# Performance work log

Hardware: AMD Instinct MI355X
Metric: run time of the kernel (lower is better)

The kernel has to match this reference:

```python
import jax, jax.numpy as jnp
import numpy as np


def _fake_quant(w):
    # Dynamic per-tensor int8 quantization of weights (scale = max|w|/127),
    # immediately dequantized, as quantized_lstm does for its packed weights.
    s = jnp.max(jnp.abs(w)) / 127.0
    q = jnp.clip(jnp.round(w / s), -128.0, 127.0) * s
    # straight-through so the same code is usable under vjp
    return w + jax.lax.stop_gradient(q - w)


def _run_dir(xs, h0, c0, w_ih, w_hh, b, reverse):
    # xs: [T,B,in]; h0,c0: [B,H]; w_ih: [4H,in]; w_hh: [4H,H]; b: [4H]
    def step(carry, x_t):
        h, c = carry
        gates = x_t @ w_ih.T + h @ w_hh.T + b  # [B,4H]
        i, f, g, o = jnp.split(gates, 4, axis=-1)  # PyTorch gate order i,f,g,o
        c = jax.nn.sigmoid(f) * c + jax.nn.sigmoid(i) * jnp.tanh(g)
        h = jax.nn.sigmoid(o) * jnp.tanh(c)
        return (h, c), h
    (hT, cT), ys = jax.lax.scan(step, (h0, c0), xs, reverse=reverse)
    return ys, hT, cT


def _lstm(x, h0, c0, w_ih, w_hh, b_ih, b_hh):
    # x: [B,T,I] (batch_first); h0/c0: [L*2,B,H]; weights stacked [L,2,...]
    L = w_ih.shape[0]
    xs = jnp.transpose(x, (1, 0, 2))  # time-major [T,B,I]
    h_n, c_n = [], []
    for l in range(L):
        outs = []
        for d in range(2):  # 0=fwd, 1=bwd
            idx = 2 * l + d
            wih = _fake_quant(w_ih[l, d])
            whh = _fake_quant(w_hh[l, d])
            b = b_ih[l, d] + b_hh[l, d]
            ys, hT, cT = _run_dir(xs, h0[idx], c0[idx], wih, whh, b, reverse=(d == 1))
            outs.append(ys)
            h_n.append(hT)
            c_n.append(cT)
        xs = jnp.concatenate(outs, axis=-1)  # [T,B,2H] feeds next layer
    out = jnp.transpose(xs, (1, 0, 2))  # back to batch_first [B,T,2H]
    return out, jnp.stack(h_n), jnp.stack(c_n)


def setup_inputs() -> dict:
    key = jax.random.key(0)
    ks = jax.random.split(key, 7)
    B, T, I, H, L = 32, 256, 1024, 512, 2
    sc = 1.0 / np.sqrt(H)
    return {
        "x": jax.random.normal(ks[0], (B, T, I), jnp.float32),
        "h0": jax.random.normal(ks[1], (2 * L, B, H), jnp.float32),
        "c0": jax.random.normal(ks[2], (2 * L, B, H), jnp.float32),
        "w_ih": jax.random.normal(ks[3], (L, 2, 4 * H, I), jnp.float32) * sc,
        "w_hh": jax.random.normal(ks[4], (L, 2, 4 * H, H), jnp.float32) * sc,
        "b_ih": jax.random.normal(ks[5], (L, 2, 4 * H), jnp.float32) * sc,
        "b_hh": jax.random.normal(ks[6], (L, 2, 4 * H), jnp.float32) * sc,
    }


def reference(x, h0, c0, w_ih, w_hh, b_ih, b_hh):
    return _lstm(x, h0, c0, w_ih, w_hh, b_ih, b_hh)
```

## Files before the change

kernel.cpp:

```cpp
#include <hip/hip_runtime.h>

typedef __attribute__((ext_vector_type(8))) short bf16x8;
typedef __attribute__((ext_vector_type(4))) float f32x4;
typedef __attribute__((ext_vector_type(4))) unsigned u32x4;

#define BB   32
#define TT   256
#define II   1024
#define HH   512
#define GG   2048
#define BT   8192

#define WS_OFF_FLAGS   0ull
#define WS_OFF_SCALES  1024ull
#define WS_MEMSET_SPAN 2048ull
#define WS_OFF_QIH     4096ull
#define QIH_BYTES      (4ull*GG*II*2)
#define WS_OFF_QHH     (WS_OFF_QIH + QIH_BYTES)
#define QHH_BYTES      (4ull*GG*HH*2)
#define WS_OFF_XBUF    (WS_OFF_QHH + QHH_BYTES)
#define XBUF_BYTES     (1ull*BT*II*2)
#define WS_OFF_YS1     (WS_OFF_XBUF + XBUF_BYTES)
#define WS_OFF_HBUF    (WS_OFF_YS1 + XBUF_BYTES)
#define HBUF_BYTES     (2ull*2*BB*HH*2)
#define WS_OFF_GX      (WS_OFF_HBUF + HBUF_BYTES)
#define GX_ELEMS       (2ull*TT*GG*BB)

__device__ __forceinline__ unsigned short f2bf(float f){
  unsigned u = __float_as_uint(f);
  u += 0x7fffu + ((u >> 16) & 1u);
  return (unsigned short)(u >> 16);
}
__device__ __forceinline__ float bf2f(unsigned short h){ return __uint_as_float(((unsigned)h) << 16); }
__device__ __forceinline__ unsigned pack2(float a, float b){ return (unsigned)f2bf(a) | ((unsigned)f2bf(b) << 16); }
__device__ __forceinline__ float sigm(float x){ return 1.0f / (1.0f + __expf(-x)); }
__device__ __forceinline__ float tanh_(float x){
  float e = __expf(-2.0f * fabsf(x));
  float t = (1.0f - e) / (1.0f + e);
  return x < 0.0f ? -t : t;
}

__device__ __forceinline__ void st_short(void* p, unsigned v){
  asm volatile("global_store_short %0, %1, off" :: "v"(p), "v"(v) : "memory");
}
__device__ __forceinline__ void st_short_coh(void* p, unsigned v){
  asm volatile("global_store_short %0, %1, off sc0 sc1" :: "v"(p), "v"(v) : "memory");
}
__device__ __forceinline__ void st_dword(void* p, float v){
  asm volatile("global_store_dword %0, %1, off" :: "v"(p), "v"(v) : "memory");
}
__device__ __forceinline__ void ld_dword(float* d, const void* p){
  asm volatile("global_load_dword %0, %1, off" : "=v"(*d) : "v"(p));
}
__device__ __forceinline__ void ld_ushort(unsigned* d, const void* p){
  asm volatile("global_load_ushort %0, %1, off" : "=v"(*d) : "v"(p));
}
__device__ __forceinline__ void ld_b128_coh(u32x4* d, const void* p){
  asm volatile("global_load_dwordx4 %0, %1, off sc0 sc1" : "=v"(*d) : "v"(p));
}
__device__ __forceinline__ void ld_b128(bf16x8* d, const void* p){
  asm volatile("global_load_dwordx4 %0, %1, off" : "=v"(*d) : "v"(p));
}
#define WAITV0() do{ asm volatile("s_waitcnt vmcnt(0)" ::: "memory"); __builtin_amdgcn_sched_barrier(0); }while(0)
#define WAITL0() do{ asm volatile("s_waitcnt lgkmcnt(0)" ::: "memory"); __builtin_amdgcn_sched_barrier(0); }while(0)

__global__ __launch_bounds__(256) void k_absmax(const float* __restrict__ wih,
                                                const float* __restrict__ whh,
                                                unsigned* __restrict__ scales_raw){
  int t = blockIdx.y;
  const float* base; size_t n;
  if (t < 4){ base = wih + (size_t)t * GG * II; n = (size_t)GG * II; }
  else      { base = whh + (size_t)(t - 4) * GG * HH; n = (size_t)GG * HH; }
  size_t gtid = (size_t)blockIdx.x * 256 + threadIdx.x;
  float m = 0.0f;
  const float4* b4 = (const float4*)base;
  size_t n4 = n >> 2;
  for (size_t i = gtid; i < n4; i += 8192){
    float4 v = b4[i];
    m = fmaxf(m, fmaxf(fmaxf(fabsf(v.x), fabsf(v.y)), fmaxf(fabsf(v.z), fabsf(v.w))));
  }
  for (int off = 32; off; off >>= 1) m = fmaxf(m, __shfl_xor(m, off));
  __shared__ float red[4];
  int w = threadIdx.x >> 6, l = threadIdx.x & 63;
  if (l == 0) red[w] = m;
  __syncthreads();
  if (threadIdx.x == 0){
    m = fmaxf(fmaxf(red[0], red[1]), fmaxf(red[2], red[3]));
    atomicMax(&scales_raw[t], __float_as_uint(m));
  }
}

__global__ __launch_bounds__(256) void k_quant_ih(const float* __restrict__ wih,
                                                  unsigned short* __restrict__ qih,
                                                  const unsigned* __restrict__ scales_raw){
  size_t i8 = (size_t)blockIdx.x * 256 + threadIdx.x;
  int t = (int)(i8 >> 18);
  size_t off = (i8 & 262143) << 3;
  float s = __uint_as_float(scales_raw[t]) / 127.0f;
  s = fmaxf(s, 1e-30f);
  const float* src = wih + ((size_t)t << 21) + off;
  float4 v0 = *(const float4*)src, v1 = *(const float4*)(src + 4);
  float q[8] = {v0.x, v0.y, v0.z, v0.w, v1.x, v1.y, v1.z, v1.w};
#pragma unroll
  for (int j = 0; j < 8; ++j) q[j] = fminf(127.0f, fmaxf(-128.0f, rintf(q[j] / s)));
  uint4 o; o.x = pack2(q[0], q[1]); o.y = pack2(q[2], q[3]); o.z = pack2(q[4], q[5]); o.w = pack2(q[6], q[7]);
  *(uint4*)(qih + ((size_t)t << 21) + off) = o;
}

__global__ __launch_bounds__(256) void k_quant_hh(const float* __restrict__ whh,
                                                  unsigned short* __restrict__ qhh,
                                                  const unsigned* __restrict__ scales_raw){
  size_t i8 = (size_t)blockIdx.x * 256 + threadIdx.x;
  int t = (int)(i8 >> 17);
  size_t o = i8 & 131071;
  int k8 = (int)(o & 63);
  int r  = (int)((o >> 6) & 63);
  int bi = (int)(o >> 12);
  int w = r >> 4, hu = (r >> 2) & 3, gt = r & 3;
  int j = gt * 512 + bi * 16 + w * 4 + hu;
  float s = __uint_as_float(scales_raw[4 + t]) / 127.0f;
  s = fmaxf(s, 1e-30f);
  const float* src = whh + ((size_t)t << 20) + (size_t)j * HH + ((size_t)k8 << 3);
  float4 v0 = *(const float4*)src, v1 = *(const float4*)(src + 4);
  float q[8] = {v0.x, v0.y, v0.z, v0.w, v1.x, v1.y, v1.z, v1.w};
#pragma unroll
  for (int jj = 0; jj < 8; ++jj) q[jj] = fminf(127.0f, fmaxf(-128.0f, rintf(q[jj] / s)));
  uint4 ov; ov.x = pack2(q[0], q[1]); ov.y = pack2(q[2], q[3]); ov.z = pack2(q[4], q[5]); ov.w = pack2(q[6], q[7]);
  *(uint4*)(qhh + ((size_t)t << 20) + (((size_t)bi * 64 + r) << 9) + ((size_t)k8 << 3)) = ov;
}

__global__ __launch_bounds__(256) void k_cvtx(const float* __restrict__ x,
                                              unsigned short* __restrict__ xbuf){
  size_t i8 = (size_t)blockIdx.x * 256 + threadIdx.x;
  size_t row = i8 >> 7;
  int c8 = (int)(i8 & 127);
  int t = (int)(row >> 5), b = (int)(row & 31);
  const float* src = x + (((size_t)b * TT + t) << 10) + ((size_t)c8 << 3);
  float4 v0 = *(const float4*)src, v1 = *(const float4*)(src + 4);
  uint4 o; o.x = pack2(v0.x, v0.y); o.y = pack2(v0.z, v0.w); o.z = pack2(v1.x, v1.y); o.w = pack2(v1.z, v1.w);
  *(uint4*)(xbuf + (row << 10) + ((size_t)c8 << 3)) = o;
}

__global__ __launch_bounds__(256) void k_gemm(const unsigned short* __restrict__ Aq,
                                              const unsigned short* __restrict__ X,
                                              float* __restrict__ gxf,
                                              unsigned short* __restrict__ gxh, int gx16,
                                              const unsigned* __restrict__ scales_raw, int sbase){
  int d = blockIdx.z;
  const unsigned short* A = Aq + ((size_t)d << 21);
  float s = __uint_as_float(scales_raw[sbase + d]) / 127.0f;
  __shared__ unsigned short As[128 * 64];
  __shared__ unsigned short Bs[128 * 64];
  int tid = threadIdx.x;
  int l = tid & 63;
  int wv = tid >> 6;
  int wr = wv >> 1, wc = wv & 1;
  int jt = blockIdx.y, mt = blockIdx.x;
  size_t arow0 = (size_t)jt * 128;
  size_t brow0 = (size_t)mt * 128;
  f32x4 acc[4][4];
  f32x4 z = {0.f, 0.f, 0.f, 0.f};
#pragma unroll
  for (int i = 0; i < 4; ++i)
#pragma unroll
    for (int j = 0; j < 4; ++j) acc[i][j] = z;

  for (int kt = 0; kt < II; kt += 64){
    __syncthreads();
#pragma unroll
    for (int p = 0; p < 4; ++p){
      int ch = p * 256 + tid;
      int r = ch >> 3; int ce = (ch & 7) << 3;
      *(uint4*)&As[r * 64 + ce] = *(const uint4*)&A[(arow0 + r) * II + kt + ce];
      *(uint4*)&Bs[r * 64 + ce] = *(const uint4*)&X[(brow0 + r) * II + kt + ce];
    }
    __syncthreads();
#pragma unroll
    for (int kk = 0; kk < 64; kk += 32){
      bf16x8 a[4], b[4];
#pragma unroll
      for (int mi = 0; mi < 4; ++mi) a[mi] = *(const bf16x8*)&As[(wr * 64 + mi * 16 + (l & 15)) * 64 + kk + (l >> 4) * 8];
#pragma unroll
      for (int ni = 0; ni < 4; ++ni) b[ni] = *(const bf16x8*)&Bs[(wc * 64 + ni * 16 + (l & 15)) * 64 + kk + (l >> 4) * 8];
#pragma unroll
      for (int mi = 0; mi < 4; ++mi)
#pragma unroll
        for (int ni = 0; ni < 4; ++ni)
          acc[mi][ni] = __builtin_amdgcn_mfma_f32_16x16x32_bf16(a[mi], b[ni], acc[mi][ni], 0, 0, 0);
    }
  }
  size_t gxbase = (size_t)d * ((size_t)TT * GG * BB);
#pragma unroll
  for (int mi = 0; mi < 4; ++mi){
    int j0 = jt * 128 + wr * 64 + mi * 16 + ((l >> 4) << 2);
#pragma unroll
    for (int ni = 0; ni < 4; ++ni){
      int m = mt * 128 + wc * 64 + ni * 16 + (l & 15);
      int t = m >> 5, bb = m & 31;
#pragma unroll
      for (int r = 0; r < 4; ++r){
        size_t o = gxbase + ((size_t)(t * GG + j0 + r) * BB + bb);
        float v = s * acc[mi][ni][r];
        if (gx16) gxh[o] = f2bf(v); else gxf[o] = v;
      }
    }
  }
}

template<int GX16>
__global__ __launch_bounds__(256) void k_scan(const unsigned short* __restrict__ qhh,
                                              const float* __restrict__ gxf,
                                              const unsigned short* __restrict__ gxh,
                                              const float* __restrict__ h0,
                                              const float* __restrict__ c0,
                                              const float* __restrict__ bih,
                                              const float* __restrict__ bhh,
                                              const unsigned* __restrict__ scales_raw,
                                              unsigned short* __restrict__ hbuf,
                                              unsigned* __restrict__ flags,
                                              int layer,
                                              unsigned short* __restrict__ ys,
                                              float* __restrict__ out){
  __shared__ unsigned short Hlds[BB * HH];
  int tid = threadIdx.x;
  int d = blockIdx.x >> 5, bi = blockIdx.x & 31;
  int w = tid >> 6, l = tid & 63;
  int ld = layer * 2 + d;
  float s_hh = __uint_as_float(scales_raw[4 + ld]) / 127.0f;

  {
    const float* h0d = h0 + ((size_t)ld << 14);
    char* hb = (char*)Hlds;
#pragma unroll
    for (int p = 0; p < 8; ++p){
      int ch = p * 256 + tid;
      int b = ch >> 6; int c8 = ch & 63;
      const float* sp = h0d + ((size_t)b << 9) + (c8 << 3);
      float4 v0 = *(const float4*)sp, v1 = *(const float4*)(sp + 4);
      u32x4 o = {pack2(v0.x, v0.y), pack2(v0.z, v0.w), pack2(v1.x, v1.y), pack2(v1.z, v1.w)};
      *(u32x4*)(hb + b * 1024 + ((c8 << 4) ^ ((b & 7) << 4))) = o;
    }
  }

  int hu = l >> 4;
  int hidden = bi * 16 + w * 4 + hu;
  int bb0 = l & 15, bb1 = 16 + (l & 15);
  float bias[4];
#pragma unroll
  for (int gt = 0; gt < 4; ++gt){
    int j = gt * 512 + hidden;
    bias[gt] = bih[(size_t)ld * GG + j] + bhh[(size_t)ld * GG + j];
  }
  float cc0 = c0[((size_t)ld * BB + bb0) * HH + hidden];
  float cc1 = c0[((size_t)ld * BB + bb1) * HH + hidden];

  int rA = w * 16 + (l & 15);
  int koffe = (l >> 4) * 8;
  const unsigned short* qsl = qhh + ((size_t)ld << 20) + ((size_t)bi << 15);
  bf16x8 afrag[16];
#pragma unroll
  for (int kk = 0; kk < 16; ++kk)
    ld_b128(&afrag[kk], qsl + (size_t)rA * 512 + kk * 32 + koffe);

  const float* gxd_f = gxf + (size_t)d * ((size_t)TT * GG * BB);
  const unsigned short* gxd_h = gxh + (size_t)d * ((size_t)TT * GG * BB);
  unsigned short* hb_d = hbuf + ((size_t)d * 2) * (BB * HH);
  unsigned* fl = flags + d * 32;

  float gxv[8]; unsigned gxu[8];
  {
    int t0 = d ? TT - 1 : 0;
    size_t base = (size_t)t0 * GG * BB;
#pragma unroll
    for (int gt = 0; gt < 4; ++gt){
      size_t o = base + (size_t)(gt * 512 + hidden) * BB;
      if (GX16){ ld_ushort(&gxu[gt * 2],     gxd_h + o + bb0);
                 ld_ushort(&gxu[gt * 2 + 1], gxd_h + o + bb1); }
      else     { ld_dword(&gxv[gt * 2],      gxd_f + o + bb0);
                 ld_dword(&gxv[gt * 2 + 1],  gxd_f + o + bb1); }
    }
  }
  WAITV0();
  __syncthreads();

  const char* hldsb = (const char*)Hlds;
  int kbyte = koffe * 2;

  for (int s = 0; s < TT; ++s){
    int t = d ? (TT - 1 - s) : s;
    f32x4 acc0 = {0.f, 0.f, 0.f, 0.f}, acc1 = {0.f, 0.f, 0.f, 0.f};
#pragma unroll
    for (int kk = 0; kk < 16; ++kk){
      int cb = kk * 64 + kbyte;
      bf16x8 b0 = *(const bf16x8*)(hldsb + bb0 * 1024 + (cb ^ ((bb0 & 7) << 4)));
      bf16x8 b1 = *(const bf16x8*)(hldsb + bb1 * 1024 + (cb ^ ((bb1 & 7) << 4)));
      acc0 = __builtin_amdgcn_mfma_f32_16x16x32_bf16(afrag[kk], b0, acc0, 0, 0, 0);
      acc1 = __builtin_amdgcn_mfma_f32_16x16x32_bf16(afrag[kk], b1, acc1, 0, 0, 0);
    }
    float g0[4], g1[4];
#pragma unroll
    for (int gt = 0; gt < 4; ++gt){
      float gx0 = GX16 ? bf2f((unsigned short)gxu[gt * 2])     : gxv[gt * 2];
      float gx1 = GX16 ? bf2f((unsigned short)gxu[gt * 2 + 1]) : gxv[gt * 2 + 1];
      g0[gt] = acc0[gt] * s_hh + gx0 + bias[gt];
      g1[gt] = acc1[gt] * s_hh + gx1 + bias[gt];
    }
    float i0 = sigm(g0[0]), f0 = sigm(g0[1]), G0 = tanh_(g0[2]), o0 = sigm(g0[3]);
    float i1 = sigm(g1[0]), f1 = sigm(g1[1]), G1 = tanh_(g1[2]), o1 = sigm(g1[3]);
    float cn0 = f0 * cc0 + i0 * G0;  cc0 = cn0;
    float cn1 = f1 * cc1 + i1 * G1;  cc1 = cn1;
    float hx0 = o0 * tanh_(cn0);
    float hx1 = o1 * tanh_(cn1);
    unsigned yh0 = f2bf(hx0), yh1 = f2bf(hx1);

    size_t ybase = (((size_t)t * BB) << 10) + (size_t)d * 512 + hidden;
    st_short(ys + ybase + ((size_t)bb0 << 10), yh0);
    st_short(ys + ybase + ((size_t)bb1 << 10), yh1);

    if (s == TT - 1){
      st_dword(out + 8388608ull + ((size_t)ld * BB + bb0) * HH + hidden, hx0);
      st_dword(out + 8388608ull + ((size_t)ld * BB + bb1) * HH + hidden, hx1);
      st_dword(out + 8454144ull + ((size_t)ld * BB + bb0) * HH + hidden, cn0);
      st_dword(out + 8454144ull + ((size_t)ld * BB + bb1) * HH + hidden, cn1);
      WAITV0();
    } else {
      unsigned short* hp = hb_d + (size_t)((s + 1) & 1) * (BB * HH);
      st_short_coh(hp + (size_t)bb0 * HH + hidden, yh0);
      st_short_coh(hp + (size_t)bb1 * HH + hidden, yh1);
      WAITV0();
      __syncthreads();
      if (tid == 0)
        __hip_atomic_store(&fl[bi], (unsigned)(s + 1), __ATOMIC_RELAXED, __HIP_MEMORY_SCOPE_AGENT);
      {
        int tn = d ? (TT - 2 - s) : (s + 1);
        size_t base = (size_t)tn * GG * BB;
#pragma unroll
        for (int gt = 0; gt < 4; ++gt){
          size_t o = base + (size_t)(gt * 512 + hidden) * BB;
          if (GX16){ ld_ushort(&gxu[gt * 2],     gxd_h + o + bb0);
                     ld_ushort(&gxu[gt * 2 + 1], gxd_h + o + bb1); }
          else     { ld_dword(&gxv[gt * 2],      gxd_f + o + bb0);
                     ld_dword(&gxv[gt * 2 + 1],  gxd_f + o + bb1); }
        }
      }
      if (tid < 32){
        unsigned target = (unsigned)(s + 1);
        while (true){
          unsigned v = __hip_atomic_load(&fl[tid], __ATOMIC_RELAXED, __HIP_MEMORY_SCOPE_AGENT);
          if (__all((int)(v >= target))) break;
          __builtin_amdgcn_s_sleep(1);
        }
      }
      __syncthreads();
      u32x4 hv[8];
      const char* srcb = (const char*)hp;
#pragma unroll
      for (int p = 0; p < 8; ++p){
        int ch = p * 256 + tid;
        int b = ch >> 6; int cb2 = (ch & 63) << 4;
        ld_b128_coh(&hv[p], srcb + b * 1024 + cb2);
      }
      WAITV0();
      char* hbw = (char*)Hlds;
#pragma unroll
      for (int p = 0; p < 8; ++p){
        int ch = p * 256 + tid;
        int b = ch >> 6; int cb2 = (ch & 63) << 4;
        *(u32x4*)(hbw + b * 1024 + (cb2 ^ ((b & 7) << 4))) = hv[p];
      }
      WAITL0();
      __builtin_amdgcn_s_barrier();
      __builtin_amdgcn_sched_barrier(0);
    }
  }
}

__global__ __launch_bounds__(256) void k_out(const unsigned short* __restrict__ ys,
                                             float* __restrict__ out){
  size_t i4 = (size_t)blockIdx.x * 256 + threadIdx.x;
  size_t idx = i4 << 2;
  size_t row = idx >> 10; int c = (int)(idx & 1023);
  int t = (int)(row >> 5), b = (int)(row & 31);
  ushort4 v = *(const ushort4*)&ys[idx];
  float4 o = {bf2f(v.x), bf2f(v.y), bf2f(v.z), bf2f(v.w)};
  *(float4*)&out[(((size_t)b * TT + t) << 10) + c] = o;
}

extern "C" void kernel_launch(void* const* d_in, const int* in_sizes, int n_in,
                              void* d_out, int out_size, void* d_ws, size_t ws_size,
                              hipStream_t stream){
  if (n_in < 7) return;
  const float* x   = (const float*)d_in[0];
  const float* h0  = (const float*)d_in[1];
  const float* c0  = (const float*)d_in[2];
  const float* wih = (const float*)d_in[3];
  const float* whh = (const float*)d_in[4];
  const float* bih = (const float*)d_in[5];
  const float* bhh = (const float*)d_in[6];
  float* out = (float*)d_out;

  char* ws = (char*)d_ws;
  unsigned* flags = (unsigned*)(ws + WS_OFF_FLAGS);
  unsigned* scales = (unsigned*)(ws + WS_OFF_SCALES);
  unsigned short* qih  = (unsigned short*)(ws + WS_OFF_QIH);
  unsigned short* qhh  = (unsigned short*)(ws + WS_OFF_QHH);
  unsigned short* xbuf = (unsigned short*)(ws + WS_OFF_XBUF);
  unsigned short* ys1  = (unsigned short*)(ws + WS_OFF_YS1);
  unsigned short* hbuf = (unsigned short*)(ws + WS_OFF_HBUF);
  float* gxf = (float*)(ws + WS_OFF_GX);
  unsigned short* gxh = (unsigned short*)(ws + WS_OFF_GX);

  size_t need_f32 = WS_OFF_GX + GX_ELEMS * 4ull;
  int gx16 = (ws_size >= need_f32) ? 0 : 1;

  (void)hipMemsetAsync(ws, 0, WS_MEMSET_SPAN, stream);

  k_absmax<<<dim3(32, 8), 256, 0, stream>>>(wih, whh, scales);
  k_quant_ih<<<4096, 256, 0, stream>>>(wih, qih, scales);
  k_quant_hh<<<2048, 256, 0, stream>>>(whh, qhh, scales);
  k_cvtx<<<4096, 256, 0, stream>>>(x, xbuf);

  k_gemm<<<dim3(64, 16, 2), 256, 0, stream>>>(qih, xbuf, gxf, gxh, gx16, scales, 0);
  if (gx16) k_scan<1><<<64, 256, 0, stream>>>(qhh, gxf, gxh, h0, c0, bih, bhh, scales, hbuf, flags, 0, ys1, out);
  else      k_scan<0><<<64, 256, 0, stream>>>(qhh, gxf, gxh, h0, c0, bih, bhh, scales, hbuf, flags, 0, ys1, out);
  k_gemm<<<dim3(64, 16, 2), 256, 0, stream>>>(qih + 2ull * GG * II, ys1, gxf, gxh, gx16, scales, 2);
  if (gx16) k_scan<1><<<64, 256, 0, stream>>>(qhh, gxf, gxh, h0, c0, bih, bhh, scales, hbuf, flags + 64, 1, ys1, out);
  else      k_scan<0><<<64, 256, 0, stream>>>(qhh, gxf, gxh, h0, c0, bih, bhh, scales, hbuf, flags + 64, 1, ys1, out);

  k_out<<<8192, 256, 0, stream>>>(ys1, out);

  (void)in_sizes; (void)out_size;
}
```

Baseline: 2.227 ms.

## Exchange hidden state as MFMA-fragment layout via global, dropping LDS staging

The scan kernel no longer copies the full hidden state into LDS each step. Each block now publishes its 16-column slice of h in a global fragment-ordered buffer, and every wave loads its MFMA B operands straight from global with coherent 128-bit loads. The h0 initialization also goes through this path, which shifts the flag numbering by one. Per-element short stores are replaced by a small LDS stage, and ys and h are written with 128-bit stores. This cuts LDS traffic and a barrier per step, but every wave now issues 32 coherent global loads per step on the serial critical path.

```diff
diff --git a/kernel.cpp b/kernel.cpp
--- a/kernel.cpp
+++ b/kernel.cpp
@@ -21,9 +21,9 @@
 #define WS_OFF_XBUF    (WS_OFF_QHH + QHH_BYTES)
 #define XBUF_BYTES     (1ull*BT*II*2)
 #define WS_OFF_YS1     (WS_OFF_XBUF + XBUF_BYTES)
-#define WS_OFF_HBUF    (WS_OFF_YS1 + XBUF_BYTES)
-#define HBUF_BYTES     (2ull*2*BB*HH*2)
-#define WS_OFF_GX      (WS_OFF_HBUF + HBUF_BYTES)
+#define WS_OFF_HFRAG   (WS_OFF_YS1 + XBUF_BYTES)
+#define HFRAG_BYTES    (2ull*2*2*16*1024)
+#define WS_OFF_GX      (WS_OFF_HFRAG + HFRAG_BYTES)
 #define GX_ELEMS       (2ull*TT*GG*BB)
 
 __device__ __forceinline__ unsigned short f2bf(float f){
@@ -40,29 +40,28 @@
   return x < 0.0f ? -t : t;
 }
 
-__device__ __forceinline__ void st_short(void* p, unsigned v){
-  asm volatile("global_store_short %0, %1, off" :: "v"(p), "v"(v) : "memory");
-}
-__device__ __forceinline__ void st_short_coh(void* p, unsigned v){
-  asm volatile("global_store_short %0, %1, off sc0 sc1" :: "v"(p), "v"(v) : "memory");
-}
 __device__ __forceinline__ void st_dword(void* p, float v){
   asm volatile("global_store_dword %0, %1, off" :: "v"(p), "v"(v) : "memory");
 }
+__device__ __forceinline__ void st_b128(void* p, u32x4 v){
+  asm volatile("global_store_dwordx4 %0, %1, off" :: "v"(p), "v"(v) : "memory");
+}
+__device__ __forceinline__ void st_b128_coh(void* p, u32x4 v){
+  asm volatile("global_store_dwordx4 %0, %1, off sc0 sc1" :: "v"(p), "v"(v) : "memory");
+}
 __device__ __forceinline__ void ld_dword(float* d, const void* p){
   asm volatile("global_load_dword %0, %1, off" : "=v"(*d) : "v"(p));
 }
 __device__ __forceinline__ void ld_ushort(unsigned* d, const void* p){
   asm volatile("global_load_ushort %0, %1, off" : "=v"(*d) : "v"(p));
 }
-__device__ __forceinline__ void ld_b128_coh(u32x4* d, const void* p){
+__device__ __forceinline__ void ld_frag(bf16x8* d, const void* p){
+  asm volatile("global_load_dwordx4 %0, %1, off" : "=v"(*d) : "v"(p));
+}
+__device__ __forceinline__ void ld_frag_coh(bf16x8* d, const void* p){
   asm volatile("global_load_dwordx4 %0, %1, off sc0 sc1" : "=v"(*d) : "v"(p));
 }
-__device__ __forceinline__ void ld_b128(bf16x8* d, const void* p){
-  asm volatile("global_load_dwordx4 %0, %1, off" : "=v"(*d) : "v"(p));
-}
 #define WAITV0() do{ asm volatile("s_waitcnt vmcnt(0)" ::: "memory"); __builtin_amdgcn_sched_barrier(0); }while(0)
-#define WAITL0() do{ asm volatile("s_waitcnt lgkmcnt(0)" ::: "memory"); __builtin_amdgcn_sched_barrier(0); }while(0)
 
 __global__ __launch_bounds__(256) void k_absmax(const float* __restrict__ wih,
                                                 const float* __restrict__ whh,
@@ -216,35 +215,41 @@
                                               const float* __restrict__ bih,
                                               const float* __restrict__ bhh,
                                               const unsigned* __restrict__ scales_raw,
-                                              unsigned short* __restrict__ hbuf,
+                                              char* __restrict__ hfrag,
                                               unsigned* __restrict__ flags,
                                               int layer,
                                               unsigned short* __restrict__ ys,
                                               float* __restrict__ out){
-  __shared__ unsigned short Hlds[BB * HH];
+  __shared__ __align__(16) unsigned short stage[512];
   int tid = threadIdx.x;
   int d = blockIdx.x >> 5, bi = blockIdx.x & 31;
   int w = tid >> 6, l = tid & 63;
   int ld = layer * 2 + d;
   float s_hh = __uint_as_float(scales_raw[4 + ld]) / 127.0f;
 
-  {
-    const float* h0d = h0 + ((size_t)ld << 14);
-    char* hb = (char*)Hlds;
-#pragma unroll
-    for (int p = 0; p < 8; ++p){
-      int ch = p * 256 + tid;
-      int b = ch >> 6; int c8 = ch & 63;
-      const float* sp = h0d + ((size_t)b << 9) + (c8 << 3);
-      float4 v0 = *(const float4*)sp, v1 = *(const float4*)(sp + 4);
-      u32x4 o = {pack2(v0.x, v0.y), pack2(v0.z, v0.w), pack2(v1.x, v1.y), pack2(v1.z, v1.w)};
-      *(u32x4*)(hb + b * 1024 + ((c8 << 4) ^ ((b & 7) << 4))) = o;
-    }
-  }
-
   int hu = l >> 4;
   int hidden = bi * 16 + w * 4 + hu;
-  int bb0 = l & 15, bb1 = 16 + (l & 15);
+  int klocal = w * 4 + hu;
+  int bb0 = l & 15, bb1 = 16 + bb0;
+
+  char* hfd = hfrag + (size_t)d * 65536;
+  unsigned* fl = flags + d * 32;
+
+  int p_arr = l >> 5, p_z = (l >> 4) & 1, p_bb = l & 15;
+  size_t p_rec = (size_t)p_arr * 16384 + (size_t)(bi >> 1) * 1024
+               + (size_t)((2 * (bi & 1) + p_z) * 16 + p_bb) * 16;
+
+  if (w == 0){
+    const float* sp = h0 + ((size_t)ld << 14) + ((size_t)(p_arr * 16 + p_bb) << 9)
+                    + bi * 16 + p_z * 8;
+    float4 v0 = *(const float4*)sp, v1 = *(const float4*)(sp + 4);
+    u32x4 o = {pack2(v0.x, v0.y), pack2(v0.z, v0.w), pack2(v1.x, v1.y), pack2(v1.z, v1.w)};
+    st_b128_coh(hfd + p_rec, o);
+    WAITV0();
+    if (tid == 0)
+      __hip_atomic_store(&fl[bi], 1u, __ATOMIC_RELAXED, __HIP_MEMORY_SCOPE_AGENT);
+  }
+
   float bias[4];
 #pragma unroll
   for (int gt = 0; gt < 4; ++gt){
@@ -260,12 +265,10 @@
   bf16x8 afrag[16];
 #pragma unroll
   for (int kk = 0; kk < 16; ++kk)
-    ld_b128(&afrag[kk], qsl + (size_t)rA * 512 + kk * 32 + koffe);
+    ld_frag(&afrag[kk], qsl + (size_t)rA * 512 + kk * 32 + koffe);
 
   const float* gxd_f = gxf + (size_t)d * ((size_t)TT * GG * BB);
   const unsigned short* gxd_h = gxh + (size_t)d * ((size_t)TT * GG * BB);
-  unsigned short* hb_d = hbuf + ((size_t)d * 2) * (BB * HH);
-  unsigned* fl = flags + d * 32;
 
   float gxv[8]; unsigned gxu[8];
   {
@@ -280,23 +283,35 @@
                  ld_dword(&gxv[gt * 2 + 1],  gxd_f + o + bb1); }
     }
   }
-  WAITV0();
-  __syncthreads();
-
-  const char* hldsb = (const char*)Hlds;
-  int kbyte = koffe * 2;
 
   for (int s = 0; s < TT; ++s){
     int t = d ? (TT - 1 - s) : s;
+
+    if (w == 0 && l < 32){
+      unsigned target = (unsigned)(s + 1);
+      while (true){
+        unsigned v = __hip_atomic_load(&fl[l], __ATOMIC_RELAXED, __HIP_MEMORY_SCOPE_AGENT);
+        if (__all((int)(v >= target))) break;
+        __builtin_amdgcn_s_sleep(1);
+      }
+    }
+    __syncthreads();
+
+    const char* pb = hfd + (size_t)(s & 1) * 32768 + (size_t)l * 16;
+    bf16x8 b0f[16], b1f[16];
+#pragma unroll
+    for (int kk = 0; kk < 16; ++kk) ld_frag_coh(&b0f[kk], pb + kk * 1024);
+#pragma unroll
+    for (int kk = 0; kk < 16; ++kk) ld_frag_coh(&b1f[kk], pb + 16384 + kk * 1024);
+    WAITV0();
+
     f32x4 acc0 = {0.f, 0.f, 0.f, 0.f}, acc1 = {0.f, 0.f, 0.f, 0.f};
 #pragma unroll
     for (int kk = 0; kk < 16; ++kk){
-      int cb = kk * 64 + kbyte;
-      bf16x8 b0 = *(const bf16x8*)(hldsb + bb0 * 1024 + (cb ^ ((bb0 & 7) << 4)));
-      bf16x8 b1 = *(const bf16x8*)(hldsb + bb1 * 1024 + (cb ^ ((bb1 & 7) << 4)));
-      acc0 = __builtin_amdgcn_mfma_f32_16x16x32_bf16(afrag[kk], b0, acc0, 0, 0, 0);
-      acc1 = __builtin_amdgcn_mfma_f32_16x16x32_bf16(afrag[kk], b1, acc1, 0, 0, 0);
-    }
+      acc0 = __builtin_amdgcn_mfma_f32_16x16x32_bf16(afrag[kk], b0f[kk], acc0, 0, 0, 0);
+      acc1 = __builtin_amdgcn_mfma_f32_16x16x32_bf16(afrag[kk], b1f[kk], acc1, 0, 0, 0);
+    }
+
     float g0[4], g1[4];
 #pragma unroll
     for (int gt = 0; gt < 4; ++gt){
@@ -311,68 +326,47 @@
     float cn1 = f1 * cc1 + i1 * G1;  cc1 = cn1;
     float hx0 = o0 * tanh_(cn0);
     float hx1 = o1 * tanh_(cn1);
-    unsigned yh0 = f2bf(hx0), yh1 = f2bf(hx1);
-
-    size_t ybase = (((size_t)t * BB) << 10) + (size_t)d * 512 + hidden;
-    st_short(ys + ybase + ((size_t)bb0 << 10), yh0);
-    st_short(ys + ybase + ((size_t)bb1 << 10), yh1);
 
     if (s == TT - 1){
       st_dword(out + 8388608ull + ((size_t)ld * BB + bb0) * HH + hidden, hx0);
       st_dword(out + 8388608ull + ((size_t)ld * BB + bb1) * HH + hidden, hx1);
       st_dword(out + 8454144ull + ((size_t)ld * BB + bb0) * HH + hidden, cn0);
       st_dword(out + 8454144ull + ((size_t)ld * BB + bb1) * HH + hidden, cn1);
-      WAITV0();
-    } else {
-      unsigned short* hp = hb_d + (size_t)((s + 1) & 1) * (BB * HH);
-      st_short_coh(hp + (size_t)bb0 * HH + hidden, yh0);
-      st_short_coh(hp + (size_t)bb1 * HH + hidden, yh1);
-      WAITV0();
-      __syncthreads();
-      if (tid == 0)
-        __hip_atomic_store(&fl[bi], (unsigned)(s + 1), __ATOMIC_RELAXED, __HIP_MEMORY_SCOPE_AGENT);
-      {
-        int tn = d ? (TT - 2 - s) : (s + 1);
-        size_t base = (size_t)tn * GG * BB;
-#pragma unroll
-        for (int gt = 0; gt < 4; ++gt){
-          size_t o = base + (size_t)(gt * 512 + hidden) * BB;
-          if (GX16){ ld_ushort(&gxu[gt * 2],     gxd_h + o + bb0);
-                     ld_ushort(&gxu[gt * 2 + 1], gxd_h + o + bb1); }
-          else     { ld_dword(&gxv[gt * 2],      gxd_f + o + bb0);
-                     ld_dword(&gxv[gt * 2 + 1],  gxd_f + o + bb1); }
-        }
+    }
+
+    stage[bb0 * 16 + klocal]       = f2bf(hx0);
+    stage[256 + bb0 * 16 + klocal] = f2bf(hx1);
+    __syncthreads();
+
+    if (w == 0){
+      if (s < TT - 1){
+        u32x4 v = *(const u32x4*)&stage[p_arr * 256 + p_bb * 16 + p_z * 8];
+        st_b128_coh(hfd + (size_t)((s + 1) & 1) * 32768 + p_rec, v);
+        WAITV0();
+        if (tid == 0)
+          __hip_atomic_store(&fl[bi], (unsigned)(s + 2), __ATOMIC_RELAXED, __HIP_MEMORY_SCOPE_AGENT);
       }
-      if (tid < 32){
-        unsigned target = (unsigned)(s + 1);
-        while (true){
-          unsigned v = __hip_atomic_load(&fl[tid], __ATOMIC_RELAXED, __HIP_MEMORY_SCOPE_AGENT);
-          if (__all((int)(v >= target))) break;
-          __builtin_amdgcn_s_sleep(1);
-        }
+    } else if (w == 1){
+      int i = tid - 64;
+      int arr = i >> 5, bbx = (i >> 1) & 15, half = i & 1;
+      u32x4 v = *(const u32x4*)&stage[arr * 256 + bbx * 16 + half * 8];
+      st_b128(ys + (((size_t)(t * BB + arr * 16 + bbx)) << 10) + d * 512 + bi * 16 + half * 8, v);
+    }
+
+    if (s < TT - 1){
+      int tn = d ? (TT - 2 - s) : (s + 1);
+      size_t base = (size_t)tn * GG * BB;
+#pragma unroll
+      for (int gt = 0; gt < 4; ++gt){
+        size_t o = base + (size_t)(gt * 512 + hidden) * BB;
+        if (GX16){ ld_ushort(&gxu[gt * 2],     gxd_h + o + bb0);
+                   ld_ushort(&gxu[gt * 2 + 1], gxd_h + o + bb1); }
+        else     { ld_dword(&gxv[gt * 2],      gxd_f + o + bb0);
+                   ld_dword(&gxv[gt * 2 + 1],  gxd_f + o + bb1); }
       }
-      __syncthreads();
-      u32x4 hv[8];
-      const char* srcb = (const char*)hp;
-#pragma unroll
-      for (int p = 0; p < 8; ++p){
-        int ch = p * 256 + tid;
-        int b = ch >> 6; int cb2 = (ch & 63) << 4;
-        ld_b128_coh(&hv[p], srcb + b * 1024 + cb2);
-      }
-      WAITV0();
-      char* hbw = (char*)Hlds;
-#pragma unroll
-      for (int p = 0; p < 8; ++p){
-        int ch = p * 256 + tid;
-        int b = ch >> 6; int cb2 = (ch & 63) << 4;
-        *(u32x4*)(hbw + b * 1024 + (cb2 ^ ((b & 7) << 4))) = hv[p];
-      }
-      WAITL0();
-      __builtin_amdgcn_s_barrier();
-      __builtin_amdgcn_sched_barrier(0);
-    }
-  }
+    }
+  }
+  WAITV0();
 }
 
 __global__ __launch_bounds__(256) void k_out(const unsigned short* __restrict__ ys,
@@ -406,7 +400,7 @@
   unsigned short* qhh  = (unsigned short*)(ws + WS_OFF_QHH);
   unsigned short* xbuf = (unsigned short*)(ws + WS_OFF_XBUF);
   unsigned short* ys1  = (unsigned short*)(ws + WS_OFF_YS1);
-  unsigned short* hbuf = (unsigned short*)(ws + WS_OFF_HBUF);
+  char* hfrag = ws + WS_OFF_HFRAG;
   float* gxf = (float*)(ws + WS_OFF_GX);
   unsigned short* gxh = (unsigned short*)(ws + WS_OFF_GX);
 
@@ -421,11 +415,11 @@
   k_cvtx<<<4096, 256, 0, stream>>>(x, xbuf);
 
   k_gemm<<<dim3(64, 16, 2), 256, 0, stream>>>(qih, xbuf, gxf, gxh, gx16, scales, 0);
-  if (gx16) k_scan<1><<<64, 256, 0, stream>>>(qhh, gxf, gxh, h0, c0, bih, bhh, scales, hbuf, flags, 0, ys1, out);
-  else      k_scan<0><<<64, 256, 0, stream>>>(qhh, gxf, gxh, h0, c0, bih, bhh, scales, hbuf, flags, 0, ys1, out);
+  if (gx16) k_scan<1><<<64, 256, 0, stream>>>(qhh, gxf, gxh, h0, c0, bih, bhh, scales, hfrag, flags, 0, ys1, out);
+  else      k_scan<0><<<64, 256, 0, stream>>>(qhh, gxf, gxh, h0, c0, bih, bhh, scales, hfrag, flags, 0, ys1, out);
   k_gemm<<<dim3(64, 16, 2), 256, 0, stream>>>(qih + 2ull * GG * II, ys1, gxf, gxh, gx16, scales, 2);
-  if (gx16) k_scan<1><<<64, 256, 0, stream>>>(qhh, gxf, gxh, h0, c0, bih, bhh, scales, hbuf, flags + 64, 1, ys1, out);
-  else      k_scan<0><<<64, 256, 0, stream>>>(qhh, gxf, gxh, h0, c0, bih, bhh, scales, hbuf, flags + 64, 1, ys1, out);
+  if (gx16) k_scan<1><<<64, 256, 0, stream>>>(qhh, gxf, gxh, h0, c0, bih, bhh, scales, hfrag, flags + 64, 1, ys1, out);
+  else      k_scan<0><<<64, 256, 0, stream>>>(qhh, gxf, gxh, h0, c0, bih, bhh, scales, hfrag, flags + 64, 1, ys1, out);
 
   k_out<<<8192, 256, 0, stream>>>(ys1, out);
 
```

Measured after the change: 2.145 ms (median of 2 runs). 1.04x faster.
